# Kernel optimization log

Hardware: AMD Instinct MI355X
Metric: run time of the kernel (lower is better)

The kernel has to match this reference:

```python
import jax, jax.numpy as jnp
import numpy as np


def lstm_cell(x, h, c, Wih, Whh, b):
    # PyTorch LSTM gate order: i, f, g, o
    z = x @ Wih.T + h @ Whh.T + b
    i, f, g, o = jnp.split(z, 4, axis=-1)
    c = jax.nn.sigmoid(f) * c + jax.nn.sigmoid(i) * jnp.tanh(g)
    h = jax.nn.sigmoid(o) * jnp.tanh(c)
    return h, c


def run_dir(xs, Wih, Whh, b, reverse):
    # xs: [S, B, D_in] -> outputs [S, B, H], final (h, c)
    B = xs.shape[1]
    H = Whh.shape[1]
    init = (jnp.zeros((B, H), xs.dtype), jnp.zeros((B, H), xs.dtype))
    def step(carry, x):
        h, c = carry
        h, c = lstm_cell(x, h, c, Wih, Whh, b)
        return (h, c), h
    (h, c), ys = jax.lax.scan(step, init, xs, reverse=reverse)
    return ys, h, c


def _p(k, shape, scale=0.05):
    return jax.random.normal(k, shape, dtype=jnp.float32) * scale


def setup_inputs():
    V, E, H = 32000, 128, 256
    B, S, T = 32, 256, 64
    ks = jax.random.split(jax.random.key(0), 24)
    return {
        "src": jax.random.randint(ks[0], (B, S), 0, V),
        "tgt": jax.random.randint(ks[1], (B, T), 0, V),
        "emb": _p(ks[2], (V, E), 1.0),
        "enc_Wih_l0": _p(ks[3], (2, 4 * H, E)),
        "enc_Whh_l0": _p(ks[4], (2, 4 * H, H)),
        "enc_b_l0": _p(ks[5], (2, 4 * H)),
        "enc_Wih_l1": _p(ks[6], (2, 4 * H, 2 * H)),
        "enc_Whh_l1": _p(ks[7], (2, 4 * H, H)),
        "enc_b_l1": _p(ks[8], (2, 4 * H)),
        "dec_Wih0": _p(ks[9], (8 * H, E + 2 * H)),
        "dec_Whh0": _p(ks[10], (8 * H, 2 * H)),
        "dec_b0": _p(ks[11], (8 * H,)),
        "dec_Wih1": _p(ks[12], (8 * H, 2 * H)),
        "dec_Whh1": _p(ks[13], (8 * H, 2 * H)),
        "dec_b1": _p(ks[14], (8 * H,)),
        "attn_W1": _p(ks[15], (H, 4 * H)),
        "attn_b1": _p(ks[16], (H,)),
        "attn_W2": _p(ks[17], (1, H)),
        "attn_b2": _p(ks[18], (1,)),
        "out_W1": _p(ks[19], (H, 2 * H)),
        "out_b1": _p(ks[20], (H,)),
        "out_W2": _p(ks[21], (V, H)),
        "out_b2": _p(ks[22], (V,)),
    }


def reference(src, tgt, emb, enc_Wih_l0, enc_Whh_l0, enc_b_l0, enc_Wih_l1, enc_Whh_l1, enc_b_l1, dec_Wih0, dec_Whh0, dec_b0, dec_Wih1, dec_Whh1, dec_b1, attn_W1, attn_b1, attn_W2, attn_b2, out_W1, out_b1, out_W2, out_b2):
    # dropout layers are identity in eval mode
    H2 = dec_Whh0.shape[1]  # 2*hidden_dim = 512
    src_e = emb[src]                        # [B, S, E]
    tgt_e = emb[tgt]                        # [B, T, E]
    xs = jnp.swapaxes(src_e, 0, 1)          # [S, B, E]

    # 2-layer bidirectional encoder
    yf, hf0, cf0 = run_dir(xs, enc_Wih_l0[0], enc_Whh_l0[0], enc_b_l0[0], False)
    yb, hb0, cb0 = run_dir(xs, enc_Wih_l0[1], enc_Whh_l0[1], enc_b_l0[1], True)
    y0 = jnp.concatenate([yf, yb], axis=-1)  # [S, B, 2H]
    yf1, hf1, cf1 = run_dir(y0, enc_Wih_l1[0], enc_Whh_l1[0], enc_b_l1[0], False)
    yb1, hb1, cb1 = run_dir(y0, enc_Wih_l1[1], enc_Whh_l1[1], enc_b_l1[1], True)
    enc_out = jnp.swapaxes(jnp.concatenate([yf1, yb1], axis=-1), 0, 1)  # [B, S, 2H]

    # decoder init: per-layer concat of fwd/bwd final states (matches the view/transpose)
    h0 = jnp.concatenate([hf0, hb0], axis=-1)
    c0 = jnp.concatenate([cf0, cb0], axis=-1)
    h1 = jnp.concatenate([hf1, hb1], axis=-1)
    c1 = jnp.concatenate([cf1, cb1], axis=-1)

    # attention: Linear(4H, H) split into decoder-hidden part and encoder part
    W1_dec = attn_W1[:, :H2]
    W1_enc = attn_W1[:, H2:]
    enc_proj = jnp.einsum('bsd,hd->bsh', enc_out, W1_enc) + attn_b1  # precompute once

    dec_xs = jnp.swapaxes(tgt_e[:, :-1, :], 0, 1)  # [T-1, B, E]

    def step(carry, x_t):
        h0, c0, h1, c1 = carry
        e = jnp.tanh(enc_proj + (h1 @ W1_dec.T)[:, None, :])  # [B, S, H]
        scores = e @ attn_W2[0] + attn_b2[0]                  # [B, S]
        a = jax.nn.softmax(scores, axis=1)
        ctx = jnp.einsum('bs,bsd->bd', a, enc_out)            # [B, 2H]
        x = jnp.concatenate([x_t, ctx], axis=-1)              # [B, E+2H]
        h0, c0 = lstm_cell(x, h0, c0, dec_Wih0, dec_Whh0, dec_b0)
        h1, c1 = lstm_cell(h0, h1, c1, dec_Wih1, dec_Whh1, dec_b1)
        hid = jax.nn.relu(h1 @ out_W1.T + out_b1)
        logits = hid @ out_W2.T + out_b2                      # [B, V]
        return (h0, c0, h1, c1), logits

    _, ys = jax.lax.scan(step, (h0, c0, h1, c1), dec_xs)      # [T-1, B, V]
    return jnp.swapaxes(ys, 0, 1)                             # [B, T-1, V]
```

## Files before the change

### kernel.cpp

```cpp
#include <hip/hip_runtime.h>

#define BB_ 32
#define SS_ 256
#define TD_ 63
#define EE_ 128
#define VV_ 32000

typedef unsigned short u16;
typedef unsigned int u32;
typedef unsigned long long u64;
typedef __attribute__((ext_vector_type(8))) short short8v;
typedef __attribute__((ext_vector_type(4))) float f32x4;

__device__ __forceinline__ float sigf(float x){ return 1.0f/(1.0f+__expf(-x)); }
__device__ __forceinline__ float tanhf_fast(float x){ return 1.0f - 2.0f/(__expf(2.0f*x)+1.0f); }
__device__ __forceinline__ u16 f2bf(float f){
  unsigned u = __float_as_uint(f);
  u += 0x7fff + ((u >> 16) & 1);
  return (u16)(u >> 16);
}
__device__ __forceinline__ u32 packbf(float a, float b){
  return (u32)f2bf(a) | ((u32)f2bf(b) << 16);
}
__device__ __forceinline__ float bflo(u32 v){ return __uint_as_float(v << 16); }
__device__ __forceinline__ float bfhi(u32 v){ return __uint_as_float(v & 0xffff0000u); }

__device__ __forceinline__ u32 aldu(const u32* p){
  return __hip_atomic_load(p, __ATOMIC_RELAXED, __HIP_MEMORY_SCOPE_AGENT);
}
__device__ __forceinline__ u64 ald64u(const u32* p){
  return __hip_atomic_load((const u64*)p, __ATOMIC_RELAXED, __HIP_MEMORY_SCOPE_AGENT);
}
__device__ __forceinline__ void astu(u32* p, u32 v){
  __hip_atomic_store(p, v, __ATOMIC_RELAXED, __HIP_MEMORY_SCOPE_AGENT);
}
__device__ __forceinline__ float aldf(const float* p){
  return __hip_atomic_load(p, __ATOMIC_RELAXED, __HIP_MEMORY_SCOPE_AGENT);
}
__device__ __forceinline__ void astf(float* p, float v){
  __hip_atomic_store(p, v, __ATOMIC_RELAXED, __HIP_MEMORY_SCOPE_AGENT);
}
__device__ __forceinline__ void vdrain(){ asm volatile("s_waitcnt vmcnt(0)" ::: "memory"); }

__device__ __forceinline__ short8v mkfrag(u64 a, u64 b){
  union { u32 u[4]; short8v v; } c;
  c.u[0] = (u32)a; c.u[1] = (u32)(a >> 32);
  c.u[2] = (u32)b; c.u[3] = (u32)(b >> 32);
  return c.v;
}

#define OFF_Z        0u
#define OFF_Y0       16777216u
#define OFF_Y1       20971520u
#define OFF_ZPRE     25165824u
#define OFF_H1ALL    29294592u
#define OFF_SRCE     30326784u
#define OFF_TGTE     31375360u
#define OFF_EPROJ    31633408u
#define OFF_ENCA0    33730560u
#define OFF_ENCA1    33992704u
#define OFF_DECA     34254848u
#define OFF_ATP      36352000u
#define OFF_E0H      36417536u
#define OFF_E0C      36433920u
#define OFF_E1H      36450304u
#define OFF_E1C      36466688u
#define OFF_H0P      36483072u
#define OFF_H1P      36499456u
#define OFF_CTXP     36515840u
#define OFF_CTXS     36532224u
#define OFF_Y1P      36532288u
#define OFF_HEXA     38629440u
#define OFF_HEXB     38645824u
#define OFF_BARS     38662208u

#define W_EPROJ   0u
#define W_ZPRE    2097152u
#define W_Y1P     6225920u
#define W_DECA    8323072u
#define W_ATP     10420224u
#define W_H0P     10485760u
#define W_H1P     10502144u
#define W_CTXP    10518528u
#define W_CTXS    10534912u
#define W_H1ALL   10534976u
#define W_HIDP    11567168u
#define W_DBAR    11829312u
#define W_TOTAL   11831360u

__device__ __forceinline__ void icbar(unsigned* ctr, unsigned target){
  vdrain();
  __syncthreads();
  if (threadIdx.x == 0){
    __hip_atomic_fetch_add(ctr, 1u, __ATOMIC_RELAXED, __HIP_MEMORY_SCOPE_AGENT);
    while (__hip_atomic_load(ctr, __ATOMIC_RELAXED, __HIP_MEMORY_SCOPE_AGENT) < target)
      __builtin_amdgcn_s_sleep(1);
  }
  __syncthreads();
  asm volatile("" ::: "memory");
}

__device__ __forceinline__ void icbar3(unsigned* db, unsigned gen, bool isRoot){
  vdrain();
  __syncthreads();
  int tid = threadIdx.x;
  unsigned g = (unsigned)blockIdx.x & 15u;
  if (tid == 0)
    __hip_atomic_fetch_add(&db[g*32], 1u, __ATOMIC_RELAXED, __HIP_MEMORY_SCOPE_AGENT);
  if (isRoot){
    if (tid < 64){
      unsigned tgt = gen * 8u;
      for (;;){
        unsigned a = (tid < 16)
          ? __hip_atomic_load(&db[(unsigned)tid*32], __ATOMIC_RELAXED, __HIP_MEMORY_SCOPE_AGENT)
          : tgt;
        if (__all(a >= tgt)) break;
        __builtin_amdgcn_s_sleep(1);
      }
      if (tid < 16)
        __hip_atomic_store(&db[512 + (unsigned)tid*32], gen, __ATOMIC_RELAXED, __HIP_MEMORY_SCOPE_AGENT);
      if (tid == 16)
        __hip_atomic_store(&db[1024], gen, __ATOMIC_RELAXED, __HIP_MEMORY_SCOPE_AGENT);
    }
  } else {
    if (tid == 0){
      while (__hip_atomic_load(&db[512 + g*32], __ATOMIC_RELAXED, __HIP_MEMORY_SCOPE_AGENT) < gen)
        __builtin_amdgcn_s_sleep(1);
    }
  }
  __syncthreads();
  asm volatile("" ::: "memory");
}

__global__ void k_zero(float* __restrict__ p, int n){
  int i = blockIdx.x*256 + threadIdx.x;
  if (i < n) p[i] = 0.f;
}

__global__ void k_gather(const int* __restrict__ src, const int* __restrict__ tgt,
                         const float* __restrict__ emb,
                         float* __restrict__ src_e, float* __restrict__ tgt_e){
  int idx = blockIdx.x*256 + threadIdx.x;
  const int total = (8192 + 2016) * 32;
  if (idx >= total) return;
  int row = idx >> 5, j = idx & 31;
  int tok; float* dst;
  if (row < 8192){
    int s = row >> 5, b = row & 31;
    tok = src[b*SS_ + s];
    dst = src_e + (size_t)row*EE_;
  } else {
    int r2 = row - 8192;
    int t = r2 >> 5, b = r2 & 31;
    tok = tgt[b*64 + t];
    dst = tgt_e + (size_t)r2*EE_;
  }
  float4 v = *(const float4*)(emb + (size_t)tok*EE_ + j*4);
  *(float4*)(dst + j*4) = v;
}

__global__ void k_prep_encA(const float* __restrict__ W, u16* __restrict__ out){
  int idx = blockIdx.x*256 + threadIdx.x;
  if (idx >= 65536) return;
  int l = idx & 63, kk = (idx>>6)&7, m = (idx>>9)&7, us = (idx>>12)&7, d = (idx>>15)&1;
  int r = l & 15, g = r & 3, ut = r >> 2;
  int gcol = g*256 + us*32 + m*4 + ut;
  int k0 = kk*32 + (l>>4)*8;
  const float* wp = W + ((size_t)d*1024 + gcol)*256 + k0;
  u16 v[8];
  #pragma unroll
  for (int j=0;j<8;j++) v[j] = f2bf(wp[j]);
  *(uint4*)(out + (size_t)idx*8) = *(uint4*)v;
}

__global__ void k_prep_decA(const float* __restrict__ Wih0, const float* __restrict__ Whh0,
                            const float* __restrict__ Wih1, const float* __restrict__ Whh1,
                            u16* __restrict__ out){
  int idx = blockIdx.x*256 + threadIdx.x;
  if (idx >= 524288) return;
  int l = idx & 63, kk = (idx>>6)&31, cell = (idx>>11)&1, B = idx>>12;
  int r = l & 15;
  int ul = r >> 2, g = r & 3;
  int gcol = g*512 + B*4 + ul;
  int k0 = kk*32 + (l>>4)*8;
  u16 v[8];
  #pragma unroll
  for (int j=0;j<8;j++){
    int k = k0 + j;
    float wv;
    if (cell == 0) wv = (k < 512) ? Wih0[(size_t)gcol*640 + 128 + k] : Whh0[(size_t)gcol*512 + k - 512];
    else           wv = (k < 512) ? Wih1[(size_t)gcol*512 + k]       : Whh1[(size_t)gcol*512 + k - 512];
    v[j] = f2bf(wv);
  }
  *(uint4*)(out + (size_t)idx*8) = *(uint4*)v;
}

__global__ void k_prep_aTp(const float* __restrict__ aW1, u32* __restrict__ aTp){
  int idx = blockIdx.x*256 + threadIdx.x;
  if (idx >= 65536) return;
  int j2 = idx >> 8, c = idx & 255;
  aTp[idx] = packbf(aW1[(size_t)c*1024 + 2*j2], aW1[(size_t)c*1024 + 2*j2 + 1]);
}

__global__ void k_dinit(const float* __restrict__ eh0, const float* __restrict__ eh1,
                        u32* __restrict__ h0p, u32* __restrict__ h1p){
  int idx = blockIdx.x*256 + threadIdx.x;
  if (idx >= 8192) return;
  int b = idx >> 8, i = idx & 255;
  int dd = (2*i) >> 8, uu = (2*i) & 255;
  const float* p0 = eh0 + ((size_t)dd*32 + b)*256 + uu;
  const float* p1 = eh1 + ((size_t)dd*32 + b)*256 + uu;
  h0p[b*256 + i] = packbf(p0[0], p0[1]);
  h1p[b*256 + i] = packbf(p1[0], p1[1]);
}

__global__ __launch_bounds__(256) void k_mgemm(
    const float* __restrict__ A, const float* __restrict__ Bm,
    const float* __restrict__ bias, float* __restrict__ C,
    int M, int N, int K, int ldb, int boff, int flags){
  __shared__ u16 As[128*72];
  __shared__ u16 Bs[128*72];
  int tid = threadIdx.x;
  int m0 = blockIdx.x*128, n0 = blockIdx.y*128;
  int l = tid & 63, w = tid >> 6;
  int wr = w >> 1, wc = w & 1;
  int lr = l & 15, lk = (l >> 4) * 8;
  f32x4 acc[4][4];
  #pragma unroll
  for (int m=0;m<4;m++)
    #pragma unroll
    for (int n=0;n<4;n++) acc[m][n] = (f32x4){0.f,0.f,0.f,0.f};

  int r = tid >> 1, half = tid & 1;
  bool aval = (m0 + r) < M;
  const float* arow = A + (size_t)(m0 + r)*K + half*32;
  const float* brow = Bm + (size_t)(n0 + r)*ldb + boff + half*32;
  u16* asd = &As[r*72 + half*32];
  u16* bsd = &Bs[r*72 + half*32];

  for (int k0 = 0; k0 < K; k0 += 64){
    #pragma unroll
    for (int j = 0; j < 4; j++){
      float4 x = make_float4(0.f,0.f,0.f,0.f), y = x;
      if (aval){
        x = *(const float4*)(arow + k0 + j*8);
        y = *(const float4*)(arow + k0 + j*8 + 4);
      }
      asd[j*8+0]=f2bf(x.x); asd[j*8+1]=f2bf(x.y); asd[j*8+2]=f2bf(x.z); asd[j*8+3]=f2bf(x.w);
      asd[j*8+4]=f2bf(y.x); asd[j*8+5]=f2bf(y.y); asd[j*8+6]=f2bf(y.z); asd[j*8+7]=f2bf(y.w);
      float4 p = *(const float4*)(brow + k0 + j*8);
      float4 q = *(const float4*)(brow + k0 + j*8 + 4);
      bsd[j*8+0]=f2bf(p.x); bsd[j*8+1]=f2bf(p.y); bsd[j*8+2]=f2bf(p.z); bsd[j*8+3]=f2bf(p.w);
      bsd[j*8+4]=f2bf(q.x); bsd[j*8+5]=f2bf(q.y); bsd[j*8+6]=f2bf(q.z); bsd[j*8+7]=f2bf(q.w);
    }
    __syncthreads();
    #pragma unroll
    for (int kk = 0; kk < 2; kk++){
      short8v aF[4], bF[4];
      #pragma unroll
      for (int m = 0; m < 4; m++)
        aF[m] = *(short8v*)&As[(wr*64 + m*16 + lr)*72 + kk*32 + lk];
      #pragma unroll
      for (int n = 0; n < 4; n++)
        bF[n] = *(short8v*)&Bs[(wc*64 + n*16 + lr)*72 + kk*32 + lk];
      #pragma unroll
      for (int m = 0; m < 4; m++)
        #pragma unroll
        for (int n = 0; n < 4; n++)
          acc[m][n] = __builtin_amdgcn_mfma_f32_16x16x32_bf16(aF[m], bF[n], acc[m][n], 0, 0, 0);
    }
    __syncthreads();
  }

  #pragma unroll
  for (int m = 0; m < 4; m++){
    int gr0 = m0 + wr*64 + m*16 + (l >> 4)*4;
    #pragma unroll
    for (int n = 0; n < 4; n++){
      int gc = n0 + wc*64 + n*16 + (l & 15);
      float bv = bias[gc];
      #pragma unroll
      for (int j = 0; j < 4; j++){
        int gr = gr0 + j;
        if (gr >= M) continue;
        float v = acc[m][n][j] + bv;
        if (flags & 1) v = fmaxf(v, 0.f);
        if (flags & 2){
          int t = gr >> 5, b = gr & 31;
          C[((size_t)(b*63 + t))*(size_t)N + gc] = v;
        } else if (flags & 4){
          int s = gr >> 5, b = gr & 31;
          C[((size_t)(b*256 + s))*(size_t)N + gc] = v;
        } else {
          C[(size_t)gr*N + gc] = v;
        }
      }
    }
  }
}

__global__ __launch_bounds__(256) void k_enc_scan(
    const float* __restrict__ Z, const u16* __restrict__ encA,
    float* __restrict__ y, u32* __restrict__ y1p,
    u32* __restrict__ hexp, float* __restrict__ hfin, float* __restrict__ cfin,
    unsigned* __restrict__ bars){
  extern __shared__ char smem[];
  char* ldsA = smem;
  int blk = blockIdx.x, tid = threadIdx.x;
  int us = blk & 7, bh = (blk>>3)&1, d = blk>>4;
  int dom = d*2 + bh;
  unsigned* ctr = bars + dom*32;
  int w = tid >> 6, l = tid & 63;
  int lr = l & 15, lk = l >> 4;
  { const uint4* s = (const uint4*)(encA + (size_t)(d*8+us)*32768);
    uint4* dst = (uint4*)ldsA;
    for (int i = tid; i < 4096; i += 256) dst[i] = s[i]; }
  float c0 = 0.f, c1 = 0.f;
  int b_g = bh*16 + lr;
  int uc0 = us*32 + w*8 + lk, uc1 = uc0 + 4;
  u32* hx = hexp + dom*4096;
  __syncthreads();
  float za[4], zb[4];
  {
    int t0 = d ? 255 : 0;
    const float* zr = Z + ((size_t)t0*32 + b_g)*2048 + d*1024;
    #pragma unroll
    for (int j = 0; j < 4; j++){ za[j] = zr[j*256 + uc0]; zb[j] = zr[j*256 + uc1]; }
  }
  for (int i = 0; i < 256; i++){
    int t = d ? (255 - i) : i;
    int par_r = (i & 1) ^ 1;
    u64 bq[16];
    const u32* bs = hx + par_r*2048 + lr*128;
    #pragma unroll
    for (int kk = 0; kk < 8; kk++){
      bq[2*kk]   = ald64u(bs + kk*16 + lk*4);
      bq[2*kk+1] = ald64u(bs + kk*16 + lk*4 + 2);
    }
    f32x4 acc0 = (f32x4){0.f,0.f,0.f,0.f};
    f32x4 acc1 = (f32x4){0.f,0.f,0.f,0.f};
    #pragma unroll
    for (int kk = 0; kk < 8; kk++){
      short8v bF = mkfrag(bq[2*kk], bq[2*kk+1]);
      short8v a0 = *(const short8v*)(ldsA + (((w*2+0)*8 + kk)*64 + l)*16);
      short8v a1 = *(const short8v*)(ldsA + (((w*2+1)*8 + kk)*64 + l)*16);
      acc0 = __builtin_amdgcn_mfma_f32_16x16x32_bf16(a0, bF, acc0, 0, 0, 0);
      acc1 = __builtin_amdgcn_mfma_f32_16x16x32_bf16(a1, bF, acc1, 0, 0, 0);
    }
    float z0 = acc0[0]+za[0], z1 = acc0[1]+za[1], z2 = acc0[2]+za[2], z3 = acc0[3]+za[3];
    float cn = sigf(z1)*c0 + sigf(z0)*tanhf_fast(z2);
    float hn0 = sigf(z3)*tanhf_fast(cn); c0 = cn;
    z0 = acc1[0]+zb[0]; z1 = acc1[1]+zb[1]; z2 = acc1[2]+zb[2]; z3 = acc1[3]+zb[3];
    cn = sigf(z1)*c1 + sigf(z0)*tanhf_fast(z2);
    float hn1 = sigf(z3)*tanhf_fast(cn); c1 = cn;
    size_t yr = ((size_t)t*32 + b_g)*512 + d*256;
    y[yr + uc0] = hn0; y[yr + uc1] = hn1;
    float p0 = __shfl_xor(hn0, 16);
    float p1 = __shfl_xor(hn1, 16);
    if ((lk & 1) == 0){
      int base = us*16 + w*4 + (lk >> 1);
      u32 pk0 = packbf(hn0, p0), pk1 = packbf(hn1, p1);
      astu(hx + (i&1)*2048 + lr*128 + base,     pk0);
      astu(hx + (i&1)*2048 + lr*128 + base + 2, pk1);
      if (y1p){
        int gb = d*128 + base;
        y1p[((size_t)t*32 + b_g)*256 + gb]     = pk0;
        y1p[((size_t)t*32 + b_g)*256 + gb + 2] = pk1;
      }
    }
    if (i == 255){
      size_t fb = ((size_t)d*32 + b_g)*256;
      hfin[fb + uc0] = hn0; hfin[fb + uc1] = hn1;
      cfin[fb + uc0] = c0;  cfin[fb + uc1] = c1;
      break;
    }
    {
      int tn = d ? (254 - i) : (i + 1);
      const float* zr = Z + ((size_t)tn*32 + b_g)*2048 + d*1024;
      #pragma unroll
      for (int j = 0; j < 4; j++){ za[j] = zr[j*256 + uc0]; zb[j] = zr[j*256 + uc1]; }
    }
    icbar(ctr, (unsigned)(i+1)*8u);
  }
}

__global__ __launch_bounds__(256) void k_dec_scan(
    const u32* __restrict__ aTp, const float* __restrict__ eproj,
    const float* __restrict__ aW2, const u32* __restrict__ y1p,
    const float* __restrict__ zpre, const float* __restrict__ db1,
    const u16* __restrict__ decA,
    const float* __restrict__ e0c, const float* __restrict__ e1c,
    u32* __restrict__ h0p, u32* __restrict__ h1p,
    u32* __restrict__ ctxp, float* __restrict__ ctxS,
    float* __restrict__ H1all, unsigned* __restrict__ bars,
    const float* __restrict__ oW1, const float* __restrict__ ob1,
    const float* __restrict__ oW2, const float* __restrict__ ob2,
    u32* __restrict__ hidp, float* __restrict__ out){
  extern __shared__ char smem[];
  int Bid = blockIdx.x, tid = threadIdx.x;

  if (Bid < 128){
    char* ldsA = smem;
    f32x4* pAc0 = (f32x4*)(smem + 65536);
    f32x4* pAc1 = (f32x4*)(smem + 65536 + 2048);
    f32x4* pB   = (f32x4*)(smem + 65536 + 4096);
    f32x4* pC   = (f32x4*)(smem + 65536 + 6144);
    float* h1s = (float*)(smem + 65536 + 8192);
    float* qs  = h1s + 512;
    float* w2s = qs + 256;
    float* es  = w2s + 256;
    int w = tid >> 6, l = tid & 63;
    int n_ = w & 1, kh = w >> 1;
    int lr = l & 15, lk = l >> 4;
    int idx = n_*64 + l;
    bool isRoot = (Bid == 127);
    { const uint4* s = (const uint4*)(decA + (size_t)Bid*32768);
      uint4* d4 = (uint4*)ldsA;
      for (int i = tid; i < 4096; i += 256) d4[i] = s[i]; }
    bool att = (Bid < 64);
    int attb = Bid >> 1, attp = Bid & 1;
    if (att) w2s[tid] = aW2[tid];
    int u = Bid*4 + lk;
    int b_e = n_*16 + lr;
    float c0r=0.f, c1r=0.f, d0=0.f, d1=0.f, d2=0.f, d3=0.f;
    if (kh == 1){
      int dd = u >> 8, uu = u & 255;
      c0r = e0c[((size_t)dd*32 + b_e)*256 + uu];
      c1r = e1c[((size_t)dd*32 + b_e)*256 + uu];
      d0 = db1[u]; d1 = db1[512+u]; d2 = db1[1024+u]; d3 = db1[1536+u];
    }
    int brow_off = (n_*16 + lr)*256;
    __syncthreads();
    unsigned gen = 0;
    for (int t = 0; t < TD_; t++){
      int hp = t & 1;
      f32x4 rA0, rA1;
      float zp0=0.f, zp1=0.f, zp2=0.f, zp3=0.f;
      {
        if (kh == 1){
          const float* zp = zpre + ((size_t)t*32 + b_e)*2048 + u;
          zp0 = zp[0]; zp1 = zp[512]; zp2 = zp[1024]; zp3 = zp[1536];
        }
        const u32* r0 = h0p + hp*8192 + brow_off;
        const u32* r1 = h1p + hp*8192 + brow_off;
        u64 qa[16], qb[16];
        #pragma unroll
        for (int k2 = 0; k2 < 8; k2++){
          int a = (kh*8 + k2)*16 + lk*4;
          qa[2*k2] = ald64u(r0 + a); qa[2*k2+1] = ald64u(r0 + a + 2);
        }
        #pragma unroll
        for (int k2 = 0; k2 < 8; k2++){
          int a = (kh*8 + k2)*16 + lk*4;
          qb[2*k2] = ald64u(r1 + a); qb[2*k2+1] = ald64u(r1 + a + 2);
        }
        f32x4 aA = (f32x4){0.f,0.f,0.f,0.f};
        f32x4 aB = (f32x4){0.f,0.f,0.f,0.f};
        #pragma unroll
        for (int k2 = 0; k2 < 8; k2++){
          short8v aF = *(const short8v*)(ldsA + (((16 + kh*8 + k2)*64) + l)*16);
          aA = __builtin_amdgcn_mfma_f32_16x16x32_bf16(aF, mkfrag(qa[2*k2], qa[2*k2+1]), aA, 0, 0, 0);
        }
        #pragma unroll
        for (int k2 = 0; k2 < 8; k2++){
          short8v aF = *(const short8v*)(ldsA + (((48 + kh*8 + k2)*64) + l)*16);
          aB = __builtin_amdgcn_mfma_f32_16x16x32_bf16(aF, mkfrag(qb[2*k2], qb[2*k2+1]), aB, 0, 0, 0);
        }
        if (kh == 0){ pAc0[idx] = aA; pAc1[idx] = aB; }
        else        { rA0 = aA; rA1 = aB; }
      }
      if (att){
        int b = attb;
        u32 hv = aldu(h1p + hp*8192 + b*256 + tid);
        h1s[2*tid] = bflo(hv); h1s[2*tid+1] = bfhi(hv);
        __syncthreads();
        float q0=0.f,q1=0.f,q2=0.f,q3=0.f;
        for (int j2 = 0; j2 < 256; j2 += 4){
          u32 w0 = aTp[(j2+0)*256 + tid];
          u32 w1 = aTp[(j2+1)*256 + tid];
          u32 w2 = aTp[(j2+2)*256 + tid];
          u32 w3 = aTp[(j2+3)*256 + tid];
          q0 += bflo(w0)*h1s[2*j2]   + bfhi(w0)*h1s[2*j2+1];
          q1 += bflo(w1)*h1s[2*j2+2] + bfhi(w1)*h1s[2*j2+3];
          q2 += bflo(w2)*h1s[2*j2+4] + bfhi(w2)*h1s[2*j2+5];
          q3 += bflo(w3)*h1s[2*j2+6] + bfhi(w3)*h1s[2*j2+7];
        }
        qs[tid] = (q0+q1)+(q2+q3);
        __syncthreads();
        int sl = tid >> 3, hc = tid & 7;
        #pragma unroll
        for (int so = 0; so < 4; so++){
          int s = attp*128 + so*32 + sl;
          const float4* ep = (const float4*)(eproj + ((size_t)attb*256 + s)*256 + hc*32);
          const float4* q4 = (const float4*)(qs + hc*32);
          const float4* w4 = (const float4*)(w2s + hc*32);
          float acc = 0.f;
          #pragma unroll
          for (int k = 0; k < 8; k++){
            float4 e = ep[k], qq = q4[k], ww = w4[k];
            acc += tanhf_fast(e.x+qq.x)*ww.x + tanhf_fast(e.y+qq.y)*ww.y
                 + tanhf_fast(e.z+qq.z)*ww.z + tanhf_fast(e.w+qq.w)*ww.w;
          }
          acc += __shfl_xor(acc, 1);
          acc += __shfl_xor(acc, 2);
          acc += __shfl_xor(acc, 4);
          if (hc == 0) es[so*32 + sl] = __expf(acc);
        }
        __syncthreads();
        float a0 = 0.f, a1 = 0.f, b0 = 0.f, b1 = 0.f, S = 0.f;
        size_t ybase = ((size_t)(attp*128)*32 + b)*256 + tid;
        #pragma unroll 8
        for (int si = 0; si < 128; si += 2){
          float e0 = es[si], e1 = es[si+1];
          u32 v0 = y1p[ybase + (size_t)si*8192];
          u32 v1 = y1p[ybase + (size_t)(si+1)*8192];
          S += e0 + e1;
          a0 += e0*bflo(v0); a1 += e0*bfhi(v0);
          b0 += e1*bflo(v1); b1 += e1*bfhi(v1);
        }
        astu(ctxp + attp*8192 + b*256 + tid, packbf(a0+b0, a1+b1));
        if (tid == 0) astf(ctxS + attp*32 + b, S);
      }
      icbar3(bars, ++gen, isRoot);
      {
        float Sa = 0.f, Sb = 0.f;
        if (kh == 1){ Sa = aldf(ctxS + b_e); Sb = aldf(ctxS + 32 + b_e); }
        const u32* rc = ctxp + kh*8192 + brow_off;
        u64 qc[32];
        #pragma unroll
        for (int kk = 0; kk < 16; kk++){
          int a = kk*16 + lk*4;
          qc[2*kk] = ald64u(rc + a); qc[2*kk+1] = ald64u(rc + a + 2);
        }
        f32x4 acc = (f32x4){0.f,0.f,0.f,0.f};
        #pragma unroll
        for (int kk = 0; kk < 16; kk++){
          short8v aF = *(const short8v*)(ldsA + ((kk*64) + l)*16);
          acc = __builtin_amdgcn_mfma_f32_16x16x32_bf16(aF, mkfrag(qc[2*kk], qc[2*kk+1]), acc, 0, 0, 0);
        }
        if (kh == 0) pB[idx] = acc;
        __syncthreads();
        if (kh == 1){
          f32x4 oc = pB[idx];
          f32x4 oh = pAc0[idx];
          float sc = 1.0f / (Sa + Sb);
          float z0 = (acc[0]+oc[0])*sc + oh[0] + rA0[0] + zp0;
          float z1 = (acc[1]+oc[1])*sc + oh[1] + rA0[1] + zp1;
          float z2 = (acc[2]+oc[2])*sc + oh[2] + rA0[2] + zp2;
          float z3 = (acc[3]+oc[3])*sc + oh[3] + rA0[3] + zp3;
          float cn = sigf(z1)*c0r + sigf(z0)*tanhf_fast(z2);
          float hn = sigf(z3)*tanhf_fast(cn);
          c0r = cn;
          float other = __shfl_xor(hn, 16);
          if ((lk & 1) == 0)
            astu(h0p + (1-hp)*8192 + b_e*256 + Bid*2 + (lk>>1), packbf(hn, other));
        }
      }
      icbar3(bars, ++gen, isRoot);
      {
        const u32* rh = h0p + (1-hp)*8192 + brow_off;
        u64 qd[16];
        #pragma unroll
        for (int k2 = 0; k2 < 8; k2++){
          int a = (kh*8 + k2)*16 + lk*4;
          qd[2*k2] = ald64u(rh + a); qd[2*k2+1] = ald64u(rh + a + 2);
        }
        f32x4 acc = (f32x4){0.f,0.f,0.f,0.f};
        #pragma unroll
        for (int k2 = 0; k2 < 8; k2++){
          short8v aF = *(const short8v*)(ldsA + (((32 + kh*8 + k2)*64) + l)*16);
          acc = __builtin_amdgcn_mfma_f32_16x16x32_bf16(aF, mkfrag(qd[2*k2], qd[2*k2+1]), acc, 0, 0, 0);
        }
        if (kh == 0) pC[idx] = acc;
        __syncthreads();
        if (kh == 1){
          f32x4 oc = pC[idx];
          f32x4 oh = pAc1[idx];
          float z0 = acc[0] + oc[0] + oh[0] + rA1[0] + d0;
          float z1 = acc[1] + oc[1] + oh[1] + rA1[1] + d1;
          float z2 = acc[2] + oc[2] + oh[2] + rA1[2] + d2;
          float z3 = acc[3] + oc[3] + oh[3] + rA1[3] + d3;
          float cn = sigf(z1)*c1r + sigf(z0)*tanhf_fast(z2);
          float hn = sigf(z3)*tanhf_fast(cn);
          c1r = cn;
          astf(&H1all[((size_t)t*32 + b_e)*512 + u], hn);
          float other = __shfl_xor(hn, 16);
          if ((lk & 1) == 0)
            astu(h1p + (1-hp)*8192 + b_e*256 + Bid*2 + (lk>>1), packbf(hn, other));
        }
      }
      icbar3(bars, ++gen, isRoot);
    }
  } else {
    u16* As = (u16*)smem;
    u16* Bs = (u16*)(smem + 128*72*2);
    int hb = Bid - 128;
    int l = tid & 63, w = tid >> 6;
    int wr = w >> 1, wc = w & 1;
    int lr16 = l & 15, lk8 = (l >> 4) * 8;
    int r = tid >> 1, half = tid & 1;
    int cp = ((hb & 7) == 0 && (hb >> 3) < 16) ? (hb >> 3) : -1;
    for (int j = hb; j < 4000; j += 128){
      int c = j / 250, n = j % 250;
      if (cp >= 0 && cp <= c){
        unsigned need = (cp == 15) ? 189u : (unsigned)(12*cp + 12);
        if (tid == 0){
          while (aldu(bars + 1024) < need) __builtin_amdgcn_s_sleep(32);
        }
        __syncthreads();
        int rows = (cp == 15) ? 96 : 128;
        const float* Hc = H1all + (size_t)cp*128*512;
        for (int n0 = 0; n0 < 256; n0 += 128){
          f32x4 acc[4][4];
          #pragma unroll
          for (int m=0;m<4;m++)
            #pragma unroll
            for (int nn=0;nn<4;nn++) acc[m][nn] = (f32x4){0.f,0.f,0.f,0.f};
          for (int k0 = 0; k0 < 512; k0 += 64){
            u16* asd = &As[r*72 + half*32];
            if (r < rows){
              const u32* ap = (const u32*)(Hc + (size_t)r*512 + k0 + half*32);
              #pragma unroll
              for (int jj = 0; jj < 16; jj++){
                u64 v2 = ald64u(ap + 2*jj);
                asd[2*jj]   = f2bf(__uint_as_float((u32)v2));
                asd[2*jj+1] = f2bf(__uint_as_float((u32)(v2>>32)));
              }
            } else {
              #pragma unroll
              for (int jj = 0; jj < 16; jj++){ asd[2*jj]=0; asd[2*jj+1]=0; }
            }
            const float* brow = oW1 + (size_t)(n0 + r)*512 + k0 + half*32;
            u16* bsd = &Bs[r*72 + half*32];
            #pragma unroll
            for (int jj = 0; jj < 4; jj++){
              float4 p = *(const float4*)(brow + jj*8);
              float4 q = *(const float4*)(brow + jj*8 + 4);
              bsd[jj*8+0]=f2bf(p.x); bsd[jj*8+1]=f2bf(p.y); bsd[jj*8+2]=f2bf(p.z); bsd[jj*8+3]=f2bf(p.w);
              bsd[jj*8+4]=f2bf(q.x); bsd[jj*8+5]=f2bf(q.y); bsd[jj*8+6]=f2bf(q.z); bsd[jj*8+7]=f2bf(q.w);
            }
            __syncthreads();
            #pragma unroll
            for (int kk = 0; kk < 2; kk++){
              short8v aF[4], bF[4];
              #pragma unroll
              for (int m = 0; m < 4; m++)
                aF[m] = *(short8v*)&As[(wr*64 + m*16 + lr16)*72 + kk*32 + lk8];
              #pragma unroll
              for (int nn = 0; nn < 4; nn++)
                bF[nn] = *(short8v*)&Bs[(wc*64 + nn*16 + lr16)*72 + kk*32 + lk8];
              #pragma unroll
              for (int m = 0; m < 4; m++)
                #pragma unroll
                for (int nn = 0; nn < 4; nn++)
                  acc[m][nn] = __builtin_amdgcn_mfma_f32_16x16x32_bf16(aF[m], bF[nn], acc[m][nn], 0, 0, 0);
            }
            __syncthreads();
          }
          #pragma unroll
          for (int m = 0; m < 4; m++){
            int gr0 = wr*64 + m*16 + (l >> 4)*4;
            #pragma unroll
            for (int nn = 0; nn < 4; nn++){
              int gc = n0 + wc*64 + nn*16 + (l & 15);
              float bv = ob1[gc];
              #pragma unroll
              for (int j4 = 0; j4 < 4; j4++){
                int gr = gr0 + j4;
                float v = fmaxf(acc[m][nn][j4] + bv, 0.f);
                float o = __shfl_xor(v, 1);
                if ((l & 1) == 0 && gr < rows)
                  astu(hidp + (size_t)cp*16384 + gr*128 + (gc>>1), packbf(v, o));
              }
            }
          }
        }
        vdrain();
        __syncthreads();
        if (tid == 0) astu(bars + 1088 + cp, 1u);
        cp = -1;
      }
      if (tid == 0){
        while (aldu(bars + 1088 + c) == 0) __builtin_amdgcn_s_sleep(16);
      }
      __syncthreads();
      int rows = (c == 15) ? 96 : 128;
      int n0g = n * 128;
      f32x4 acc[4][4];
      #pragma unroll
      for (int m=0;m<4;m++)
        #pragma unroll
        for (int nn=0;nn<4;nn++) acc[m][nn] = (f32x4){0.f,0.f,0.f,0.f};
      const u32* hc = hidp + (size_t)c*16384;
      for (int k0 = 0; k0 < 256; k0 += 64){
        u32* asd32 = (u32*)&As[r*72 + half*32];
        if (r < rows){
          const u32* ap = hc + r*128 + (k0>>1) + half*16;
          #pragma unroll
          for (int jj = 0; jj < 8; jj++){
            u64 v2 = ald64u(ap + 2*jj);
            asd32[2*jj] = (u32)v2; asd32[2*jj+1] = (u32)(v2>>32);
          }
        } else {
          #pragma unroll
          for (int jj = 0; jj < 8; jj++){ asd32[2*jj]=0; asd32[2*jj+1]=0; }
        }
        const float* brow = oW2 + (size_t)(n0g + r)*256 + k0 + half*32;
        u16* bsd = &Bs[r*72 + half*32];
        #pragma unroll
        for (int jj = 0; jj < 4; jj++){
          float4 p = *(const float4*)(brow + jj*8);
          float4 q = *(const float4*)(brow + jj*8 + 4);
          bsd[jj*8+0]=f2bf(p.x); bsd[jj*8+1]=f2bf(p.y); bsd[jj*8+2]=f2bf(p.z); bsd[jj*8+3]=f2bf(p.w);
          bsd[jj*8+4]=f2bf(q.x); bsd[jj*8+5]=f2bf(q.y); bsd[jj*8+6]=f2bf(q.z); bsd[jj*8+7]=f2bf(q.w);
        }
        __syncthreads();
        #pragma unroll
        for (int kk = 0; kk < 2; kk++){
          short8v aF[4], bF[4];
          #pragma unroll
          for (int m = 0; m < 4; m++)
            aF[m] = *(short8v*)&As[(wr*64 + m*16 + lr16)*72 + kk*32 + lk8];
          #pragma unroll
          for (int nn = 0; nn < 4; nn++)
            bF[nn] = *(short8v*)&Bs[(wc*64 + nn*16 + lr16)*72 + kk*32 + lk8];
          #pragma unroll
          for (int m = 0; m < 4; m++)
            #pragma unroll
            for (int nn = 0; nn < 4; nn++)
              acc[m][nn] = __builtin_amdgcn_mfma_f32_16x16x32_bf16(aF[m], bF[nn], acc[m][nn], 0, 0, 0);
        }
        __syncthreads();
      }
      #pragma unroll
      for (int m = 0; m < 4; m++){
        int gr0 = wr*64 + m*16 + (l >> 4)*4;
        #pragma unroll
        for (int nn = 0; nn < 4; nn++){
          int gc = n0g + wc*64 + nn*16 + (l & 15);
          float bv = ob2[gc];
          #pragma unroll
          for (int j4 = 0; j4 < 4; j4++){
            int gr = gr0 + j4;
            if (gr < rows){
              int gt = c*4 + (gr >> 5), b = gr & 31;
              out[((size_t)(b*63 + gt))*(size_t)VV_ + gc] = acc[m][nn][j4] + bv;
            }
          }
        }
      }
    }
  }
}

extern "C" void kernel_launch(void* const* d_in, const int* in_sizes, int n_in,
                              void* d_out, int out_size, void* d_ws, size_t ws_size,
                              hipStream_t stream){
  (void)in_sizes; (void)n_in; (void)out_size;
  const int*   src   = (const int*)d_in[0];
  const int*   tgt   = (const int*)d_in[1];
  const float* emb   = (const float*)d_in[2];
  const float* eWih0 = (const float*)d_in[3];
  const float* eWhh0 = (const float*)d_in[4];
  const float* eb0   = (const float*)d_in[5];
  const float* eWih1 = (const float*)d_in[6];
  const float* eWhh1 = (const float*)d_in[7];
  const float* eb1   = (const float*)d_in[8];
  const float* dWih0 = (const float*)d_in[9];
  const float* dWhh0 = (const float*)d_in[10];
  const float* db0   = (const float*)d_in[11];
  const float* dWih1 = (const float*)d_in[12];
  const float* dWhh1 = (const float*)d_in[13];
  const float* db1   = (const float*)d_in[14];
  const float* aW1   = (const float*)d_in[15];
  const float* ab1   = (const float*)d_in[16];
  const float* aW2   = (const float*)d_in[17];
  const float* oW1   = (const float*)d_in[19];
  const float* ob1   = (const float*)d_in[20];
  const float* oW2   = (const float*)d_in[21];
  const float* ob2   = (const float*)d_in[22];

  float* F = (float*)d_out;
  float* W = (float*)d_ws;
  bool fused = (ws_size >= (size_t)48*1024*1024);

  float* Z     = F + OFF_Z;
  float* y0    = F + OFF_Y0;
  float* y1    = F + OFF_Y1;
  float* srcE  = F + OFF_SRCE;
  float* tgtE  = F + OFF_TGTE;
  u16*   encA0 = (u16*)(F + OFF_ENCA0);
  u16*   encA1 = (u16*)(F + OFF_ENCA1);
  float* e0h   = F + OFF_E0H;
  float* e0c   = F + OFF_E0C;
  float* e1h   = F + OFF_E1H;
  float* e1c   = F + OFF_E1C;
  u32*   hexA  = (u32*)(F + OFF_HEXA);
  u32*   hexB  = (u32*)(F + OFF_HEXB);
  unsigned* bars = (unsigned*)(F + OFF_BARS);

  float* zpre  = fused ? (W + W_ZPRE)  : (F + OFF_ZPRE);
  float* H1    = fused ? (W + W_H1ALL) : (F + OFF_H1ALL);
  float* eproj = fused ? (W + W_EPROJ) : (F + OFF_EPROJ);
  u16*   decA  = fused ? (u16*)(W + W_DECA) : (u16*)(F + OFF_DECA);
  u32*   aTp   = fused ? (u32*)(W + W_ATP)  : (u32*)(F + OFF_ATP);
  u32*   h0p   = fused ? (u32*)(W + W_H0P)  : (u32*)(F + OFF_H0P);
  u32*   h1p   = fused ? (u32*)(W + W_H1P)  : (u32*)(F + OFF_H1P);
  u32*   ctxp  = fused ? (u32*)(W + W_CTXP) : (u32*)(F + OFF_CTXP);
  float* ctxS  = fused ? (W + W_CTXS)       : (F + OFF_CTXS);
  u32*   y1p   = fused ? (u32*)(W + W_Y1P)  : (u32*)(F + OFF_Y1P);
  unsigned* dbars = fused ? (unsigned*)(W + W_DBAR) : (bars + 256);
  u32*   hidp  = fused ? (u32*)(W + W_HIDP) : (u32*)d_ws;
  float* hid   = (float*)d_ws;

  hipFuncSetAttribute((const void*)k_enc_scan, hipFuncAttributeMaxDynamicSharedMemorySize, 65536);
  hipFuncSetAttribute((const void*)k_dec_scan, hipFuncAttributeMaxDynamicSharedMemorySize, 78336);

  k_zero<<<135,256,0,stream>>>(F + OFF_HEXA, 34304);
  if (fused) k_zero<<<8,256,0,stream>>>(W + W_DBAR, 2048);
  k_gather<<<((8192+2016)*32+255)/256,256,0,stream>>>(src, tgt, emb, srcE, tgtE);
  k_prep_encA<<<256,256,0,stream>>>(eWhh0, encA0);
  k_prep_encA<<<256,256,0,stream>>>(eWhh1, encA1);
  k_prep_decA<<<2048,256,0,stream>>>(dWih0, dWhh0, dWih1, dWhh1, decA);
  k_prep_aTp<<<256,256,0,stream>>>(aW1, aTp);

  k_mgemm<<<dim3(64,16),256,0,stream>>>(srcE, eWih0, eb0, Z, 8192,2048,128, 128,0,0);
  k_enc_scan<<<32,256,65536,stream>>>(Z, encA0, y0, (u32*)nullptr, hexA, e0h, e0c, bars);
  k_mgemm<<<dim3(64,16),256,0,stream>>>(y0, eWih1, eb1, Z, 8192,2048,512, 512,0,0);
  k_enc_scan<<<32,256,65536,stream>>>(Z, encA1, y1, y1p, hexB, e1h, e1c, bars + 128);

  k_mgemm<<<dim3(64,2),256,0,stream>>>(y1, aW1, ab1, eproj, 8192,256,512, 1024,512,4);
  k_mgemm<<<dim3(16,16),256,0,stream>>>(tgtE, dWih0, db0, zpre, 2016,2048,128, 640,0,0);
  k_dinit<<<32,256,0,stream>>>(e0h, e1h, h0p, h1p);

  int decBlocks = fused ? 256 : 128;
  k_dec_scan<<<decBlocks,256,78336,stream>>>(aTp, eproj, aW2, y1p, zpre, db1, decA,
                                             e0c, e1c, h0p, h1p, ctxp, ctxS, H1, dbars,
                                             oW1, ob1, oW2, ob2, hidp, F);

  if (!fused){
    k_mgemm<<<dim3(16,2),256,0,stream>>>(H1, oW1, ob1, hid, 2016,256,512, 512,0,1);
    k_mgemm<<<dim3(16,250),256,0,stream>>>(hid, oW2, ob2, F, 2016,32000,256, 256,0,2);
  }
}
```

Measured before the change: 4.473 ms.

## Shrink encoder scan to 4 blocks per direction covering full batch

Restructures the encoder LSTM scan so that each direction uses 4 blocks instead of 16. Each block owns 64 hidden units for all 32 batch rows and holds 128KB of bf16 recurrent weights in LDS. This reduces the number of participants in the per-step inter-block barrier, and each wave now issues more MFMAs per step. Z loads are no longer prefetched a step ahead, and the higher LDS use limits each block to a single CU. The decoder's output GEMM blocks also now wait on a progress counter before starting, which could delay that work or free resources for the scan.

```diff
diff --git a/kernel.cpp b/kernel.cpp
--- a/kernel.cpp
+++ b/kernel.cpp
@@ -162,11 +162,11 @@
 __global__ void k_prep_encA(const float* __restrict__ W, u16* __restrict__ out){
   int idx = blockIdx.x*256 + threadIdx.x;
   if (idx >= 65536) return;
-  int l = idx & 63, kk = (idx>>6)&7, m = (idx>>9)&7, us = (idx>>12)&7, d = (idx>>15)&1;
-  int r = l & 15, g = r & 3, ut = r >> 2;
-  int gcol = g*256 + us*32 + m*4 + ut;
+  int l = idx & 63, kk = (idx>>6)&7, mt = (idx>>9)&15, q = (idx>>13)&3, d = (idx>>15)&1;
+  int r = l & 15, g = r & 3, ur = r >> 2;
+  int col = g*256 + q*64 + mt*4 + ur;
   int k0 = kk*32 + (l>>4)*8;
-  const float* wp = W + ((size_t)d*1024 + gcol)*256 + k0;
+  const float* wp = W + ((size_t)d*1024 + col)*256 + k0;
   u16 v[8];
   #pragma unroll
   for (int j=0;j<8;j++) v[j] = f2bf(wp[j]);
@@ -307,80 +307,87 @@
   extern __shared__ char smem[];
   char* ldsA = smem;
   int blk = blockIdx.x, tid = threadIdx.x;
-  int us = blk & 7, bh = (blk>>3)&1, d = blk>>4;
-  int dom = d*2 + bh;
-  unsigned* ctr = bars + dom*32;
+  int q = blk & 3, d = blk >> 2;
+  unsigned* ctr = bars + d*32;
   int w = tid >> 6, l = tid & 63;
   int lr = l & 15, lk = l >> 4;
-  { const uint4* s = (const uint4*)(encA + (size_t)(d*8+us)*32768);
+  { const uint4* s = (const uint4*)(encA + (size_t)(d*4+q)*65536);
     uint4* dst = (uint4*)ldsA;
-    for (int i = tid; i < 4096; i += 256) dst[i] = s[i]; }
-  float c0 = 0.f, c1 = 0.f;
-  int b_g = bh*16 + lr;
-  int uc0 = us*32 + w*8 + lk, uc1 = uc0 + 4;
-  u32* hx = hexp + dom*4096;
+    for (int i = tid; i < 8192; i += 256) dst[i] = s[i]; }
+  float creg[4][2];
+  #pragma unroll
+  for (int s=0;s<4;s++){ creg[s][0]=0.f; creg[s][1]=0.f; }
+  u32* hx = hexp + d*8192;
   __syncthreads();
-  float za[4], zb[4];
-  {
-    int t0 = d ? 255 : 0;
-    const float* zr = Z + ((size_t)t0*32 + b_g)*2048 + d*1024;
-    #pragma unroll
-    for (int j = 0; j < 4; j++){ za[j] = zr[j*256 + uc0]; zb[j] = zr[j*256 + uc1]; }
-  }
   for (int i = 0; i < 256; i++){
     int t = d ? (255 - i) : i;
     int par_r = (i & 1) ^ 1;
-    u64 bq[16];
-    const u32* bs = hx + par_r*2048 + lr*128;
+    u64 bq[2][16];
+    #pragma unroll
+    for (int bh = 0; bh < 2; bh++){
+      const u32* bs = hx + par_r*4096 + (bh*16 + lr)*128;
+      #pragma unroll
+      for (int kk = 0; kk < 8; kk++){
+        bq[bh][2*kk]   = ald64u(bs + kk*16 + lk*4);
+        bq[bh][2*kk+1] = ald64u(bs + kk*16 + lk*4 + 2);
+      }
+    }
+    float zv[4][2][4];
+    #pragma unroll
+    for (int s = 0; s < 4; s++){
+      int ug = q*64 + w*16 + s*4 + lk;
+      #pragma unroll
+      for (int bh = 0; bh < 2; bh++){
+        const float* zr = Z + ((size_t)t*32 + bh*16 + lr)*2048 + d*1024 + ug;
+        #pragma unroll
+        for (int g = 0; g < 4; g++) zv[s][bh][g] = zr[g*256];
+      }
+    }
+    f32x4 acc[4][2];
+    #pragma unroll
+    for (int s=0;s<4;s++){
+      acc[s][0] = (f32x4){0.f,0.f,0.f,0.f};
+      acc[s][1] = (f32x4){0.f,0.f,0.f,0.f};
+    }
     #pragma unroll
     for (int kk = 0; kk < 8; kk++){
-      bq[2*kk]   = ald64u(bs + kk*16 + lk*4);
-      bq[2*kk+1] = ald64u(bs + kk*16 + lk*4 + 2);
-    }
-    f32x4 acc0 = (f32x4){0.f,0.f,0.f,0.f};
-    f32x4 acc1 = (f32x4){0.f,0.f,0.f,0.f};
+      short8v b0 = mkfrag(bq[0][2*kk], bq[0][2*kk+1]);
+      short8v b1 = mkfrag(bq[1][2*kk], bq[1][2*kk+1]);
+      #pragma unroll
+      for (int s = 0; s < 4; s++){
+        short8v aF = *(const short8v*)(ldsA + (((w*4+s)*8 + kk)*64 + l)*16);
+        acc[s][0] = __builtin_amdgcn_mfma_f32_16x16x32_bf16(aF, b0, acc[s][0], 0, 0, 0);
+        acc[s][1] = __builtin_amdgcn_mfma_f32_16x16x32_bf16(aF, b1, acc[s][1], 0, 0, 0);
+      }
+    }
     #pragma unroll
-    for (int kk = 0; kk < 8; kk++){
-      short8v bF = mkfrag(bq[2*kk], bq[2*kk+1]);
-      short8v a0 = *(const short8v*)(ldsA + (((w*2+0)*8 + kk)*64 + l)*16);
-      short8v a1 = *(const short8v*)(ldsA + (((w*2+1)*8 + kk)*64 + l)*16);
-      acc0 = __builtin_amdgcn_mfma_f32_16x16x32_bf16(a0, bF, acc0, 0, 0, 0);
-      acc1 = __builtin_amdgcn_mfma_f32_16x16x32_bf16(a1, bF, acc1, 0, 0, 0);
-    }
-    float z0 = acc0[0]+za[0], z1 = acc0[1]+za[1], z2 = acc0[2]+za[2], z3 = acc0[3]+za[3];
-    float cn = sigf(z1)*c0 + sigf(z0)*tanhf_fast(z2);
-    float hn0 = sigf(z3)*tanhf_fast(cn); c0 = cn;
-    z0 = acc1[0]+zb[0]; z1 = acc1[1]+zb[1]; z2 = acc1[2]+zb[2]; z3 = acc1[3]+zb[3];
-    cn = sigf(z1)*c1 + sigf(z0)*tanhf_fast(z2);
-    float hn1 = sigf(z3)*tanhf_fast(cn); c1 = cn;
-    size_t yr = ((size_t)t*32 + b_g)*512 + d*256;
-    y[yr + uc0] = hn0; y[yr + uc1] = hn1;
-    float p0 = __shfl_xor(hn0, 16);
-    float p1 = __shfl_xor(hn1, 16);
-    if ((lk & 1) == 0){
-      int base = us*16 + w*4 + (lk >> 1);
-      u32 pk0 = packbf(hn0, p0), pk1 = packbf(hn1, p1);
-      astu(hx + (i&1)*2048 + lr*128 + base,     pk0);
-      astu(hx + (i&1)*2048 + lr*128 + base + 2, pk1);
-      if (y1p){
-        int gb = d*128 + base;
-        y1p[((size_t)t*32 + b_g)*256 + gb]     = pk0;
-        y1p[((size_t)t*32 + b_g)*256 + gb + 2] = pk1;
-      }
-    }
-    if (i == 255){
-      size_t fb = ((size_t)d*32 + b_g)*256;
-      hfin[fb + uc0] = hn0; hfin[fb + uc1] = hn1;
-      cfin[fb + uc0] = c0;  cfin[fb + uc1] = c1;
-      break;
-    }
-    {
-      int tn = d ? (254 - i) : (i + 1);
-      const float* zr = Z + ((size_t)tn*32 + b_g)*2048 + d*1024;
-      #pragma unroll
-      for (int j = 0; j < 4; j++){ za[j] = zr[j*256 + uc0]; zb[j] = zr[j*256 + uc1]; }
-    }
-    icbar(ctr, (unsigned)(i+1)*8u);
+    for (int s = 0; s < 4; s++){
+      int ug = q*64 + w*16 + s*4 + lk;
+      int pi = q*32 + w*8 + s*2 + (lk >> 1);
+      #pragma unroll
+      for (int bh = 0; bh < 2; bh++){
+        int b = bh*16 + lr;
+        float z0 = acc[s][bh][0] + zv[s][bh][0];
+        float z1 = acc[s][bh][1] + zv[s][bh][1];
+        float z2 = acc[s][bh][2] + zv[s][bh][2];
+        float z3 = acc[s][bh][3] + zv[s][bh][3];
+        float cn = sigf(z1)*creg[s][bh] + sigf(z0)*tanhf_fast(z2);
+        float hn = sigf(z3)*tanhf_fast(cn);
+        creg[s][bh] = cn;
+        y[((size_t)t*32 + b)*512 + d*256 + ug] = hn;
+        float partner = __shfl_xor(hn, 16);
+        if ((lk & 1) == 0){
+          u32 pk = packbf(hn, partner);
+          astu(hx + (i&1)*4096 + b*128 + pi, pk);
+          if (y1p) y1p[((size_t)t*32 + b)*256 + d*128 + pi] = pk;
+        }
+        if (i == 255){
+          size_t fb = ((size_t)d*32 + b)*256 + ug;
+          hfin[fb] = hn; cfin[fb] = cn;
+        }
+      }
+    }
+    if (i < 255) icbar(ctr, (unsigned)(i+1)*4u);
   }
 }
 
@@ -600,6 +607,10 @@
     int lr16 = l & 15, lk8 = (l >> 4) * 8;
     int r = tid >> 1, half = tid & 1;
     int cp = ((hb & 7) == 0 && (hb >> 3) < 16) ? (hb >> 3) : -1;
+    if (tid == 0){
+      while (aldu(bars + 1024) < 126u) __builtin_amdgcn_s_sleep(127);
+    }
+    __syncthreads();
     for (int j = hb; j < 4000; j += 128){
       int c = j / 250, n = j % 250;
       if (cp >= 0 && cp <= c){
@@ -813,7 +824,7 @@
   u32*   hidp  = fused ? (u32*)(W + W_HIDP) : (u32*)d_ws;
   float* hid   = (float*)d_ws;
 
-  hipFuncSetAttribute((const void*)k_enc_scan, hipFuncAttributeMaxDynamicSharedMemorySize, 65536);
+  hipFuncSetAttribute((const void*)k_enc_scan, hipFuncAttributeMaxDynamicSharedMemorySize, 131072);
   hipFuncSetAttribute((const void*)k_dec_scan, hipFuncAttributeMaxDynamicSharedMemorySize, 78336);
 
   k_zero<<<135,256,0,stream>>>(F + OFF_HEXA, 34304);
@@ -825,9 +836,9 @@
   k_prep_aTp<<<256,256,0,stream>>>(aW1, aTp);
 
   k_mgemm<<<dim3(64,16),256,0,stream>>>(srcE, eWih0, eb0, Z, 8192,2048,128, 128,0,0);
-  k_enc_scan<<<32,256,65536,stream>>>(Z, encA0, y0, (u32*)nullptr, hexA, e0h, e0c, bars);
+  k_enc_scan<<<8,256,131072,stream>>>(Z, encA0, y0, (u32*)nullptr, hexA, e0h, e0c, bars);
   k_mgemm<<<dim3(64,16),256,0,stream>>>(y0, eWih1, eb1, Z, 8192,2048,512, 512,0,0);
-  k_enc_scan<<<32,256,65536,stream>>>(Z, encA1, y1, y1p, hexB, e1h, e1c, bars + 128);
+  k_enc_scan<<<8,256,131072,stream>>>(Z, encA1, y1, y1p, hexB, e1h, e1c, bars + 128);
 
   k_mgemm<<<dim3(64,2),256,0,stream>>>(y1, aW1, ab1, eproj, 8192,256,512, 1024,512,4);
   k_mgemm<<<dim3(16,16),256,0,stream>>>(tgtE, dWih0, db0, zpre, 2016,2048,128, 640,0,0);
```

New measurement: 8.353 ms. 86.8% more time.
